# Kernel tuning notes

Measured on AMD Instinct MI355X. Metric: run time of the kernel, lower is better.

## Reference

```python
import jax, jax.numpy as jnp
import numpy as np

EPS = 1e-12
TEMPERATURE = 0.1
QUEUE_SIZE = 1024
CUTOFF_KM = 25.0
EARTH_R_KM = 6371.0088


def _normalize(x, axis=-1):
    n = jnp.linalg.norm(x, axis=axis, keepdims=True)
    return x / jnp.maximum(n, EPS)


def _haversine_km(a, b):
    # a: (B,1,2), b: (1,S,2) in degrees (lat, lon) -> (B,S) km
    ra, rb = jnp.deg2rad(a), jnp.deg2rad(b)
    dlat = rb[..., 0] - ra[..., 0]
    dlon = rb[..., 1] - ra[..., 1]
    h = jnp.sin(dlat / 2) ** 2 + jnp.cos(ra[..., 0]) * jnp.cos(rb[..., 0]) * jnp.sin(dlon / 2) ** 2
    return 2.0 * EARTH_R_KM * jnp.arcsin(jnp.sqrt(jnp.clip(h, 0.0, 1.0)))


def setup_inputs() -> dict:
    key = jax.random.key(0)
    k1, k2, k3, k4, k5 = jax.random.split(key, 5)
    A, B, F, S = 3, 256, 512, 100000
    V = jax.random.normal(k1, (A, B, F), dtype=jnp.float32)
    L = jax.random.normal(k2, (B, F), dtype=jnp.float32)
    # gps as (lat, lon) degrees
    gps = jax.random.uniform(k3, (B, 2), dtype=jnp.float32) * jnp.array([120.0, 360.0]) - jnp.array([60.0, 180.0])
    support_feats = jax.random.normal(k4, (S, F), dtype=jnp.float32)
    support_gps = jax.random.uniform(k5, (S, 2), dtype=jnp.float32) * jnp.array([120.0, 360.0]) - jnp.array([60.0, 180.0])
    return {"V": V, "L": L, "gps": gps, "support_feats": support_feats, "support_gps": support_gps}


def reference(V, L, gps, support_feats, support_gps):
    T, Q = TEMPERATURE, QUEUE_SIZE
    L_norm = _normalize(L, axis=1)                      # (B,F)
    org = _normalize(V[0] * L_norm, axis=1)             # (B,F)
    aug = _normalize(V[1:] * L_norm, axis=2)            # (A-1,B,F)

    # nearest_neighbours (no_grad): per-batch NN in support set by dot-product sim
    sims = jnp.einsum('sf,bf->sb', support_feats, org)  # (S,B)
    nn_idx = jnp.argmax(sims, axis=0)                   # (B,)
    nn = _normalize(support_feats[nn_idx], axis=1)      # (B,F)
    nn = jax.lax.stop_gradient(nn)

    pos = jnp.exp(jnp.einsum('abf,bf->ab', aug, nn) / T)  # (A-1,B)
    batch_den = jnp.sum(pos, axis=0)                       # (B,)

    # nn_negative_queue (no_grad): first Q support rows farther than 25 km, zeros if fewer
    dist = _haversine_km(gps[:, None, :], support_gps[None, :, :])  # (B,S)
    far = dist > CUTOFF_KM                                          # (B,S)
    order = jnp.argsort(jnp.logical_not(far), axis=1)[:, :Q]        # stable: far rows first, in order
    valid = jnp.take_along_axis(far, order, axis=1)                 # (B,Q)
    negq = jnp.where(valid[..., None], support_feats[order], 0.0)   # (B,Q,F)
    negq = jax.lax.stop_gradient(_normalize(negq, axis=2))          # zero rows stay zero

    queue_den = jnp.sum(jnp.exp(jnp.einsum('bqf,bf->bq', negq, nn) / T), axis=1)  # (B,)

    loss = jnp.mean(-batch_den / (batch_den + queue_den))
    return loss
```

## Files before the change

kernel.cpp:

```cpp
#include <hip/hip_runtime.h>
#include <hip/hip_bf16.h>
#include <math.h>

#define B_N 256
#define F_N 512
#define S_N 100000
#define Q_N 1024
#define EPSF 1e-12f
#define BM 128
#define NBLK ((S_N + BM - 1) / BM)

typedef __attribute__((ext_vector_type(8))) short short8v;
typedef __attribute__((ext_vector_type(4))) float f32x4;

__device__ __forceinline__ unsigned short f2bf(float x) {
  unsigned u = __float_as_uint(x);
  u = u + 0x7FFFu + ((u >> 16) & 1u);
  return (unsigned short)(u >> 16);
}
__device__ __forceinline__ float bf2f(unsigned short h) {
  return __uint_as_float(((unsigned)h) << 16);
}

__device__ __forceinline__ float warpReduceSum(float v) {
  #pragma unroll
  for (int o = 32; o > 0; o >>= 1) v += __shfl_down(v, o);
  return v;
}

__device__ __forceinline__ float blockReduceSum256(float v, float* buf) {
  v = warpReduceSum(v);
  int lane = threadIdx.x & 63, w = threadIdx.x >> 6;
  __syncthreads();
  if (lane == 0) buf[w] = v;
  __syncthreads();
  return buf[0] + buf[1] + buf[2] + buf[3];
}

__device__ __forceinline__ void async_copy16(void* lds, const void* g) {
  __builtin_amdgcn_global_load_lds(
      (const __attribute__((address_space(1))) unsigned int*)g,
      (__attribute__((address_space(3))) unsigned int*)lds, 16, 0, 0);
}

__device__ __forceinline__ void cvt8(const float4 a, const float4 b,
                                     short8v& hi, short8v& lo) {
  union { unsigned u[4]; short8v v; } H, L;
  float xs[8] = {a.x, a.y, a.z, a.w, b.x, b.y, b.z, b.w};
  #pragma unroll
  for (int i = 0; i < 4; ++i) {
    float p = xs[2 * i], q = xs[2 * i + 1];
    union { __hip_bfloat162 b2; unsigned u; } c;
    c.b2 = __float22bfloat162_rn(make_float2(p, q));
    H.u[i] = c.u;
    float rp = p - __uint_as_float(c.u << 16);
    float rq = q - __uint_as_float(c.u & 0xFFFF0000u);
    union { __hip_bfloat162 b2; unsigned u; } d;
    d.b2 = __float22bfloat162_rn(make_float2(rp, rq));
    L.u[i] = d.u;
  }
  hi = H.v; lo = L.v;
}

__global__ __launch_bounds__(256) void k_prep(const float* __restrict__ V,
    const float* __restrict__ L, unsigned short* __restrict__ orgst,
    float* __restrict__ aug) {
  __shared__ float buf[4];
  int b = blockIdx.x, t = threadIdx.x;
  const float2 lv = *(const float2*)&L[b * F_N + t * 2];
  float ss = blockReduceSum256(lv.x * lv.x + lv.y * lv.y, buf);
  float invL = 1.0f / fmaxf(sqrtf(ss), EPSF);
  float lnx = lv.x * invL, lny = lv.y * invL;
  #pragma unroll
  for (int a = 0; a < 3; ++a) {
    const float2 vv = *(const float2*)&V[(a * B_N + b) * F_N + t * 2];
    float yx = vv.x * lnx, yy = vv.y * lny;
    float s2 = blockReduceSum256(yx * yx + yy * yy, buf);
    float inv = 1.0f / fmaxf(sqrtf(s2), EPSF);
    if (a == 0) {
      float ox = yx * inv, oy = yy * inv;
      int f = t * 2;
      int kt = f >> 5, kk = f & 31, sub = kk >> 3, pos = kk & 7;
      unsigned short hx = f2bf(ox), hy = f2bf(oy);
      unsigned short lx = f2bf(ox - bf2f(hx)), ly = f2bf(oy - bf2f(hy));
      int base = kt * 16384 + b * 64;
      ushort2 hv; hv.x = hx; hv.y = hy;
      ushort2 lw; lw.x = lx; lw.y = ly;
      *(ushort2*)&orgst[base + ((sub ^ (b & 7)) << 3) + pos] = hv;
      *(ushort2*)&orgst[base + (((sub | 4) ^ (b & 7)) << 3) + pos] = lw;
    } else {
      float* dst = &aug[((a - 1) * B_N + b) * F_N + t * 2];
      dst[0] = yx * inv;
      dst[1] = yy * inv;
    }
  }
}

__global__ __launch_bounds__(256, 2) void k_sims(const float* __restrict__ support,
    const unsigned short* __restrict__ orgst, unsigned long long* __restrict__ keys) {
  __shared__ __align__(16) unsigned char smem[65536];

  int t = threadIdx.x;
  int lane = t & 63, w = t >> 6;
  int r15 = lane & 15, ks = lane >> 4;
  int s0 = blockIdx.x * BM;

  f32x4 acc0[16], acc1[16];
  #pragma unroll
  for (int n = 0; n < 16; ++n) {
    acc0[n] = (f32x4){0.f, 0.f, 0.f, 0.f};
    acc1[n] = (f32x4){0.f, 0.f, 0.f, 0.f};
  }

  int row0 = s0 + w * 32 + r15;
  int row1 = row0 + 16;
  if (row0 > S_N - 1) row0 = S_N - 1;
  if (row1 > S_N - 1) row1 = S_N - 1;
  const float* ap0 = support + (size_t)row0 * F_N + ks * 8;
  const float* ap1 = support + (size_t)row1 * F_N + ks * 8;

  const unsigned char* bsrc = (const unsigned char*)orgst + t * 16;
  unsigned char* bdst0 = smem + t * 16;

  #pragma unroll
  for (int p = 0; p < 8; ++p) async_copy16(bdst0 + p * 4096, bsrc + p * 4096);
  __builtin_amdgcn_sched_barrier(0);
  float4 a0a = *(const float4*)(ap0);
  float4 a0b = *(const float4*)(ap0 + 4);
  float4 a1a = *(const float4*)(ap1);
  float4 a1b = *(const float4*)(ap1 + 4);
  __builtin_amdgcn_sched_barrier(0);
  asm volatile("s_waitcnt vmcnt(4)" ::: "memory");
  __builtin_amdgcn_s_barrier();
  __builtin_amdgcn_sched_barrier(0);

  const int hioff = (ks ^ (r15 & 7)) << 4;
  const int looff = ((ks | 4) ^ (r15 & 7)) << 4;

  #pragma unroll 1
  for (int kt = 0; kt < 16; ++kt) {
    const int cur = kt & 1;
    unsigned char* bbuf = smem + cur * 32768;
    short8v ah0, al0, ah1, al1;
    cvt8(a0a, a0b, ah0, al0);
    cvt8(a1a, a1b, ah1, al1);
    if (kt < 15) {
      const unsigned char* src = bsrc + (kt + 1) * 32768;
      unsigned char* dst = smem + (cur ^ 1) * 32768 + t * 16;
      #pragma unroll
      for (int p = 0; p < 8; ++p) async_copy16(dst + p * 4096, src + p * 4096);
      __builtin_amdgcn_sched_barrier(0);
      a0a = *(const float4*)(ap0 + (kt + 1) * 32);
      a0b = *(const float4*)(ap0 + (kt + 1) * 32 + 4);
      a1a = *(const float4*)(ap1 + (kt + 1) * 32);
      a1b = *(const float4*)(ap1 + (kt + 1) * 32 + 4);
      __builtin_amdgcn_sched_barrier(0);
    }
    const unsigned char* bp = bbuf + r15 * 128 + hioff;
    const unsigned char* bq = bbuf + r15 * 128 + looff;
    #pragma unroll
    for (int n = 0; n < 16; ++n) {
      short8v bh = *(const short8v*)(bp + n * 2048);
      short8v bl = *(const short8v*)(bq + n * 2048);
      acc0[n] = __builtin_amdgcn_mfma_f32_16x16x32_bf16(ah0, bh, acc0[n], 0, 0, 0);
      acc1[n] = __builtin_amdgcn_mfma_f32_16x16x32_bf16(ah1, bh, acc1[n], 0, 0, 0);
      acc0[n] = __builtin_amdgcn_mfma_f32_16x16x32_bf16(al0, bh, acc0[n], 0, 0, 0);
      acc1[n] = __builtin_amdgcn_mfma_f32_16x16x32_bf16(al1, bh, acc1[n], 0, 0, 0);
      acc0[n] = __builtin_amdgcn_mfma_f32_16x16x32_bf16(ah0, bl, acc0[n], 0, 0, 0);
      acc1[n] = __builtin_amdgcn_mfma_f32_16x16x32_bf16(ah1, bl, acc1[n], 0, 0, 0);
    }
    if (kt < 15) {
      __builtin_amdgcn_sched_barrier(0);
      asm volatile("s_waitcnt vmcnt(4)" ::: "memory");
      __builtin_amdgcn_s_barrier();
      __builtin_amdgcn_sched_barrier(0);
    } else {
      __syncthreads();
    }
  }

  unsigned long long* wk = (unsigned long long*)smem;
  #pragma unroll
  for (int n = 0; n < 16; ++n) {
    float bv = -INFINITY;
    int bi = 0x7FFFFFFF;
    #pragma unroll
    for (int r = 0; r < 4; ++r) {
      int sA = s0 + w * 32 + ks * 4 + r;
      float vA = acc0[n][r];
      if (sA < S_N && (vA > bv || (vA == bv && sA < bi))) { bv = vA; bi = sA; }
      int sB = sA + 16;
      float vB = acc1[n][r];
      if (sB < S_N && (vB > bv || (vB == bv && sB < bi))) { bv = vB; bi = sB; }
    }
    #pragma unroll
    for (int mask = 16; mask <= 32; mask <<= 1) {
      float ov = __shfl_xor(bv, mask);
      int oi = __shfl_xor(bi, mask);
      if (ov > bv || (ov == bv && oi < bi)) { bv = ov; bi = oi; }
    }
    if (lane < 16) {
      unsigned u = __float_as_uint(bv);
      u = (u & 0x80000000u) ? ~u : (u | 0x80000000u);
      wk[w * 256 + n * 16 + lane] =
          ((unsigned long long)u << 32) |
          (unsigned long long)(0xFFFFFFFFu - (unsigned)bi);
    }
  }
  __syncthreads();
  {
    unsigned long long k0 = wk[t], k1 = wk[256 + t];
    unsigned long long k2 = wk[512 + t], k3 = wk[768 + t];
    unsigned long long m01 = k0 > k1 ? k0 : k1;
    unsigned long long m23 = k2 > k3 ? k2 : k3;
    atomicMax(&keys[t], m01 > m23 ? m01 : m23);
  }
}

__global__ __launch_bounds__(256) void k_nn(const float* __restrict__ support,
    const unsigned long long* __restrict__ keys, const float* __restrict__ aug,
    float* __restrict__ nn, float* __restrict__ bden) {
  __shared__ float buf[4];
  int b = blockIdx.x, t = threadIdx.x;
  int idx = (int)(0xFFFFFFFFu - (unsigned)(keys[b] & 0xFFFFFFFFull));
  const float2 rv = *(const float2*)&support[(size_t)idx * F_N + t * 2];
  float ss = blockReduceSum256(rv.x * rv.x + rv.y * rv.y, buf);
  float inv = 1.0f / fmaxf(sqrtf(ss), EPSF);
  float nx = rv.x * inv, ny = rv.y * inv;
  nn[b * F_N + t * 2] = nx;
  nn[b * F_N + t * 2 + 1] = ny;
  const float2 a0 = *(const float2*)&aug[(0 * B_N + b) * F_N + t * 2];
  const float2 a1 = *(const float2*)&aug[(1 * B_N + b) * F_N + t * 2];
  float d0 = blockReduceSum256(a0.x * nx + a0.y * ny, buf);
  float d1 = blockReduceSum256(a1.x * nx + a1.y * ny, buf);
  if (t == 0) bden[b] = expf(d0 * 10.0f) + expf(d1 * 10.0f);
}

__global__ __launch_bounds__(256) void k_qdot(const float* __restrict__ support,
    const float* __restrict__ gps, const float* __restrict__ sgps,
    const float* __restrict__ nn, double* __restrict__ qpart) {
  __shared__ float nns[F_N];
  __shared__ int qi[256];
  __shared__ int wtot[4];
  __shared__ double wacc[4];
  int b = blockIdx.x >> 2, c = blockIdx.x & 3;
  int t = threadIdx.x;
  int lane = t & 63, w = t >> 6;

  *(float2*)&nns[t * 2] = *(const float2*)&nn[b * F_N + t * 2];

  const float DEG2RAD = 0.017453292519943295f;
  float la = gps[b * 2] * DEG2RAD;
  float lo = gps[b * 2 + 1] * DEG2RAD;
  float ca = cosf(la);
  double xd = 25.0 / (2.0 * 6371.0088);
  float hcut = (float)(sin(xd) * sin(xd));

  int cnt = 0;
  int qlo = c * 256;
  for (int base = 0; base < S_N; base += 256) {
    int s = base + t;
    bool far = false;
    if (s < S_N) {
      float lb = sgps[s * 2] * DEG2RAD;
      float ob = sgps[s * 2 + 1] * DEG2RAD;
      float sl = sinf((lb - la) * 0.5f);
      float so = sinf((ob - lo) * 0.5f);
      float h = sl * sl + ca * cosf(lb) * so * so;
      far = h > hcut;
    }
    unsigned long long m = __ballot(far);
    if (lane == 0) wtot[w] = (int)__popcll(m);
    __syncthreads();
    int offs = cnt;
    for (int wi = 0; wi < w; ++wi) offs += wtot[wi];
    if (far) {
      int pos = offs + (int)__popcll(m & ((1ull << lane) - 1ull));
      int rel = pos - qlo;
      if (rel >= 0 && rel < 256) qi[rel] = s;
    }
    cnt += wtot[0] + wtot[1] + wtot[2] + wtot[3];
    __syncthreads();
    if (cnt >= Q_N) break;
  }
  int nvalid = cnt < Q_N ? cnt : Q_N;
  __syncthreads();

  double acc = 0.0;
  for (int j = 0; j < 64; ++j) {
    int q = qlo + w * 64 + j;
    if (q >= nvalid) break;
    int row = qi[w * 64 + j];
    const float4* rp = (const float4*)&support[(size_t)row * F_N + lane * 8];
    float4 r0 = rp[0], r1 = rp[1];
    const float4 n0 = *(const float4*)&nns[lane * 8];
    const float4 n1 = *(const float4*)&nns[lane * 8 + 4];
    float dot = r0.x * n0.x + r0.y * n0.y + r0.z * n0.z + r0.w * n0.w +
                r1.x * n1.x + r1.y * n1.y + r1.z * n1.z + r1.w * n1.w;
    float ssq = r0.x * r0.x + r0.y * r0.y + r0.z * r0.z + r0.w * r0.w +
                r1.x * r1.x + r1.y * r1.y + r1.z * r1.z + r1.w * r1.w;
    #pragma unroll
    for (int o = 32; o > 0; o >>= 1) {
      dot += __shfl_xor(dot, o);
      ssq += __shfl_xor(ssq, o);
    }
    float val = dot / fmaxf(sqrtf(ssq), EPSF);
    acc += (double)expf(val * 10.0f);
  }
  if (lane == 0) wacc[w] = acc;
  __syncthreads();
  if (t == 0) {
    int got = nvalid - qlo;
    if (got < 0) got = 0; if (got > 256) got = 256;
    int inval = 256 - got;
    qpart[blockIdx.x] = wacc[0] + wacc[1] + wacc[2] + wacc[3] + (double)inval;
  }
}

__global__ __launch_bounds__(256) void k_final(const double* __restrict__ qpart,
    const float* __restrict__ bden, float* __restrict__ out) {
  __shared__ double buf[4];
  int t = threadIdx.x;
  double qd = qpart[t * 4] + qpart[t * 4 + 1] + qpart[t * 4 + 2] + qpart[t * 4 + 3];
  double bd = (double)bden[t];
  double v = -bd / (bd + qd);
  #pragma unroll
  for (int o = 32; o > 0; o >>= 1) v += __shfl_down(v, o);
  if ((t & 63) == 0) buf[t >> 6] = v;
  __syncthreads();
  if (t == 0) out[0] = (float)((buf[0] + buf[1] + buf[2] + buf[3]) / 256.0);
}

extern "C" void kernel_launch(void* const* d_in, const int* in_sizes, int n_in,
                              void* d_out, int out_size, void* d_ws, size_t ws_size,
                              hipStream_t stream) {
  const float* V = (const float*)d_in[0];
  const float* L = (const float*)d_in[1];
  const float* gps = (const float*)d_in[2];
  const float* support = (const float*)d_in[3];
  const float* sgps = (const float*)d_in[4];
  float* out = (float*)d_out;

  char* ws = (char*)d_ws;
  unsigned long long* keys = (unsigned long long*)ws;
  float* bden = (float*)(ws + 2048);
  double* qpart = (double*)(ws + 4096);
  unsigned short* orgst = (unsigned short*)(ws + 12288);
  float* aug = (float*)(ws + 12288 + 524288);
  float* nn = (float*)(ws + 12288 + 524288 + 1048576);

  hipMemsetAsync(keys, 0, 256 * sizeof(unsigned long long), stream);
  k_prep<<<256, 256, 0, stream>>>(V, L, orgst, aug);
  k_sims<<<NBLK, 256, 0, stream>>>(support, orgst, keys);
  k_nn<<<256, 256, 0, stream>>>(support, keys, aug, nn, bden);
  k_qdot<<<1024, 256, 0, stream>>>(support, gps, sgps, nn, qpart);
  k_final<<<1, 256, 0, stream>>>(qpart, bden, out);
}
```

Before: 167.6 us.

## Split similarity GEMM over batch halves to raise occupancy; fold key reset into prep

The support-vs-batch similarity kernel now launches twice as many blocks, each covering half of the batch columns. Each block holds half the accumulators and half the shared-memory B tile, and launch bounds go from 2 to 4 blocks per SM so more waves can hide latency. The MFMA loop is wrapped in s_setprio to favour matrix issue. The key memset is moved into the prep kernel to drop one launch. The cost is that every support row (the A operand) is now read and converted to bf16 twice, once per batch half.

```diff
diff --git a/kernel.cpp b/kernel.cpp
--- a/kernel.cpp
+++ b/kernel.cpp
@@ -64,9 +64,10 @@
 
 __global__ __launch_bounds__(256) void k_prep(const float* __restrict__ V,
     const float* __restrict__ L, unsigned short* __restrict__ orgst,
-    float* __restrict__ aug) {
+    float* __restrict__ aug, unsigned long long* __restrict__ keys) {
   __shared__ float buf[4];
   int b = blockIdx.x, t = threadIdx.x;
+  if (t == 0) keys[b] = 0ull;
   const float2 lv = *(const float2*)&L[b * F_N + t * 2];
   float ss = blockReduceSum256(lv.x * lv.x + lv.y * lv.y, buf);
   float invL = 1.0f / fmaxf(sqrtf(ss), EPSF);
@@ -96,18 +97,20 @@
   }
 }
 
-__global__ __launch_bounds__(256, 2) void k_sims(const float* __restrict__ support,
+__global__ __launch_bounds__(256, 4) void k_sims(const float* __restrict__ support,
     const unsigned short* __restrict__ orgst, unsigned long long* __restrict__ keys) {
-  __shared__ __align__(16) unsigned char smem[65536];
+  __shared__ __align__(16) unsigned char smem[32768];
 
   int t = threadIdx.x;
   int lane = t & 63, w = t >> 6;
   int r15 = lane & 15, ks = lane >> 4;
-  int s0 = blockIdx.x * BM;
-
-  f32x4 acc0[16], acc1[16];
-  #pragma unroll
-  for (int n = 0; n < 16; ++n) {
+  int bid = blockIdx.x;
+  int half = (bid >= NBLK) ? 1 : 0;
+  int s0 = (half ? bid - NBLK : bid) * BM;
+
+  f32x4 acc0[8], acc1[8];
+  #pragma unroll
+  for (int n = 0; n < 8; ++n) {
     acc0[n] = (f32x4){0.f, 0.f, 0.f, 0.f};
     acc1[n] = (f32x4){0.f, 0.f, 0.f, 0.f};
   }
@@ -119,11 +122,14 @@
   const float* ap0 = support + (size_t)row0 * F_N + ks * 8;
   const float* ap1 = support + (size_t)row1 * F_N + ks * 8;
 
-  const unsigned char* bsrc = (const unsigned char*)orgst + t * 16;
-  unsigned char* bdst0 = smem + t * 16;
-
-  #pragma unroll
-  for (int p = 0; p < 8; ++p) async_copy16(bdst0 + p * 4096, bsrc + p * 4096);
+  const unsigned char* bsrc =
+      (const unsigned char*)orgst + half * 16384 + t * 16;
+
+  {
+    unsigned char* dst = smem + t * 16;
+    #pragma unroll
+    for (int p = 0; p < 4; ++p) async_copy16(dst + p * 4096, bsrc + p * 4096);
+  }
   __builtin_amdgcn_sched_barrier(0);
   float4 a0a = *(const float4*)(ap0);
   float4 a0b = *(const float4*)(ap0 + 4);
@@ -139,16 +145,15 @@
 
   #pragma unroll 1
   for (int kt = 0; kt < 16; ++kt) {
-    const int cur = kt & 1;
-    unsigned char* bbuf = smem + cur * 32768;
+    unsigned char* bbuf = smem + (kt & 1) * 16384;
     short8v ah0, al0, ah1, al1;
     cvt8(a0a, a0b, ah0, al0);
     cvt8(a1a, a1b, ah1, al1);
     if (kt < 15) {
       const unsigned char* src = bsrc + (kt + 1) * 32768;
-      unsigned char* dst = smem + (cur ^ 1) * 32768 + t * 16;
+      unsigned char* dst = smem + ((kt + 1) & 1) * 16384 + t * 16;
       #pragma unroll
-      for (int p = 0; p < 8; ++p) async_copy16(dst + p * 4096, src + p * 4096);
+      for (int p = 0; p < 4; ++p) async_copy16(dst + p * 4096, src + p * 4096);
       __builtin_amdgcn_sched_barrier(0);
       a0a = *(const float4*)(ap0 + (kt + 1) * 32);
       a0b = *(const float4*)(ap0 + (kt + 1) * 32 + 4);
@@ -158,8 +163,9 @@
     }
     const unsigned char* bp = bbuf + r15 * 128 + hioff;
     const unsigned char* bq = bbuf + r15 * 128 + looff;
-    #pragma unroll
-    for (int n = 0; n < 16; ++n) {
+    __builtin_amdgcn_s_setprio(1);
+    #pragma unroll
+    for (int n = 0; n < 8; ++n) {
       short8v bh = *(const short8v*)(bp + n * 2048);
       short8v bl = *(const short8v*)(bq + n * 2048);
       acc0[n] = __builtin_amdgcn_mfma_f32_16x16x32_bf16(ah0, bh, acc0[n], 0, 0, 0);
@@ -169,19 +175,20 @@
       acc0[n] = __builtin_amdgcn_mfma_f32_16x16x32_bf16(ah0, bl, acc0[n], 0, 0, 0);
       acc1[n] = __builtin_amdgcn_mfma_f32_16x16x32_bf16(ah1, bl, acc1[n], 0, 0, 0);
     }
+    __builtin_amdgcn_s_setprio(0);
+    __builtin_amdgcn_sched_barrier(0);
     if (kt < 15) {
-      __builtin_amdgcn_sched_barrier(0);
       asm volatile("s_waitcnt vmcnt(4)" ::: "memory");
       __builtin_amdgcn_s_barrier();
-      __builtin_amdgcn_sched_barrier(0);
     } else {
       __syncthreads();
     }
+    __builtin_amdgcn_sched_barrier(0);
   }
 
   unsigned long long* wk = (unsigned long long*)smem;
   #pragma unroll
-  for (int n = 0; n < 16; ++n) {
+  for (int n = 0; n < 8; ++n) {
     float bv = -INFINITY;
     int bi = 0x7FFFFFFF;
     #pragma unroll
@@ -202,18 +209,18 @@
     if (lane < 16) {
       unsigned u = __float_as_uint(bv);
       u = (u & 0x80000000u) ? ~u : (u | 0x80000000u);
-      wk[w * 256 + n * 16 + lane] =
+      wk[w * 128 + n * 16 + lane] =
           ((unsigned long long)u << 32) |
           (unsigned long long)(0xFFFFFFFFu - (unsigned)bi);
     }
   }
   __syncthreads();
-  {
-    unsigned long long k0 = wk[t], k1 = wk[256 + t];
-    unsigned long long k2 = wk[512 + t], k3 = wk[768 + t];
+  if (t < 128) {
+    unsigned long long k0 = wk[t], k1 = wk[128 + t];
+    unsigned long long k2 = wk[256 + t], k3 = wk[384 + t];
     unsigned long long m01 = k0 > k1 ? k0 : k1;
     unsigned long long m23 = k2 > k3 ? k2 : k3;
-    atomicMax(&keys[t], m01 > m23 ? m01 : m23);
+    atomicMax(&keys[half * 128 + t], m01 > m23 ? m01 : m23);
   }
 }
 
@@ -349,9 +356,8 @@
   float* aug = (float*)(ws + 12288 + 524288);
   float* nn = (float*)(ws + 12288 + 524288 + 1048576);
 
-  hipMemsetAsync(keys, 0, 256 * sizeof(unsigned long long), stream);
-  k_prep<<<256, 256, 0, stream>>>(V, L, orgst, aug);
-  k_sims<<<NBLK, 256, 0, stream>>>(support, orgst, keys);
+  k_prep<<<256, 256, 0, stream>>>(V, L, orgst, aug, keys);
+  k_sims<<<2 * NBLK, 256, 0, stream>>>(support, orgst, keys);
   k_nn<<<256, 256, 0, stream>>>(support, keys, aug, nn, bden);
   k_qdot<<<1024, 256, 0, stream>>>(support, gps, sgps, nn, qpart);
   k_final<<<1, 256, 0, stream>>>(qpart, bden, out);
```

New measurement: 159.7 us, median of 2. -4.7%, faster.
